# Kernel tuning notes

Measured on AMD Instinct MI355X. Metric: run time of the kernel, lower is better.

Reference implementation:

```python
import jax, jax.numpy as jnp
import numpy as np

N_ATOMS = 30000
N_PAIRS = 1200000
N_BASIS = 7
N_RADIAL = 5
N_SPECIES = 119
R_MIN = 0.5
R_MAX = 6.0
UNITS = (512, 512)
BOX = 6.0  # Angstrom box edge so many pairs fall inside the cutoff
N_FEAT = 360  # gaussian-moment feature count for n_radial=5

# static triangular index sets (fully symmetric contractions)
_TRI2_I, _TRI2_J = np.triu_indices(N_RADIAL)
_TRI3 = np.array([(i, j, k) for i in range(N_RADIAL)
                  for j in range(i, N_RADIAL)
                  for k in range(j, N_RADIAL)], dtype=np.int32)


def setup_inputs() -> dict:
    key = jax.random.key(0)
    ks = jax.random.split(key, 8)
    R = jax.random.uniform(ks[0], (N_ATOMS, 3), jnp.float32) * BOX
    Z = jax.random.randint(ks[1], (N_ATOMS,), 0, N_SPECIES, dtype=jnp.int32)
    idx = jax.random.randint(ks[2], (2, N_PAIRS), 0, N_ATOMS, dtype=jnp.int32)
    W_radial = jax.random.normal(ks[3], (N_SPECIES, N_SPECIES, N_RADIAL, N_BASIS), jnp.float32) / np.sqrt(N_BASIS)
    w1 = jax.random.normal(ks[4], (N_FEAT, UNITS[0]), jnp.float32) / np.sqrt(N_FEAT)
    b1 = jnp.zeros((UNITS[0],), jnp.float32)
    w2 = jax.random.normal(ks[5], (UNITS[0], UNITS[1]), jnp.float32) / np.sqrt(UNITS[0])
    b2 = jnp.zeros((UNITS[1],), jnp.float32)
    w3 = jax.random.normal(ks[6], (UNITS[1], 1), jnp.float32) / np.sqrt(UNITS[1])
    b3 = jnp.zeros((1,), jnp.float32)
    scale = 2.0 * jnp.ones((N_SPECIES, 1), jnp.float32)
    shift = 1.0 * jnp.ones((N_SPECIES, 1), jnp.float32)
    return dict(R=R, Z=Z, idx=idx, W_radial=W_radial, w1=w1, b1=b1,
                w2=w2, b2=b2, w3=w3, b3=b3, scale=scale, shift=shift)


def _descriptor(R, Z, idx, W_radial):
    idx_i, idx_j = idx[0], idx[1]
    # pairwise displacement (free-space displacement fn)
    dr_vec = R[idx_j] - R[idx_i]                                  # [P,3]
    dr = jnp.sqrt(jnp.sum(dr_vec * dr_vec, axis=-1) + 1e-12)      # [P]
    dn = dr_vec / (dr + 1e-5)[:, None]                            # unit vectors [P,3]

    # gaussian radial basis
    betta = N_BASIS ** 2 / R_MAX ** 2
    rad_norm = (2.0 * betta / np.pi) ** 0.25
    shifts = R_MIN + (R_MAX - R_MIN) / N_BASIS * jnp.arange(N_BASIS, dtype=jnp.float32)
    basis = rad_norm * jnp.exp(-betta * (dr[:, None] - shifts) ** 2)  # [P,B]

    # cosine cutoff and per species-pair embedding of the basis
    cutoff = 0.5 * (jnp.cos(jnp.pi * dr / R_MAX) + 1.0) * (dr < R_MAX)
    coeffs = W_radial[Z[idx_i], Z[idx_j]]                          # [P,K,B] irregular gather
    radial = jnp.einsum('pkb,pb->pk', coeffs, basis)               # [P,K]
    radial = radial * (cutoff / np.sqrt(N_BASIS))[:, None]

    seg = lambda x: jax.ops.segment_sum(x, idx_i, num_segments=N_ATOMS)
    # geometric moments of order 0..3
    m0 = seg(radial)                                               # [A,K]
    m1 = seg(radial[:, :, None] * dn[:, None, :])                  # [A,K,3]
    dn2 = dn[:, :, None] * dn[:, None, :]                          # [P,3,3]
    m2 = seg(radial[:, :, None, None] * dn2[:, None])              # [A,K,3,3]
    dn3 = dn2[:, :, :, None] * dn[:, None, None, :]                # [P,3,3,3]
    m3 = seg(radial[:, :, None, None, None] * dn3[:, None])        # [A,K,3,3,3]

    # gaussian-moment invariant contractions
    c1 = jnp.einsum('ari,asi->ars', m1, m1)
    c2 = jnp.einsum('arij,asij->ars', m2, m2)
    c3 = jnp.einsum('arijk,asijk->ars', m3, m3)
    c4 = jnp.einsum('arij,asik,atjk->arst', m2, m2, m2)
    c5 = jnp.einsum('ari,asj,atij->arst', m1, m1, m2)
    c6 = jnp.einsum('arijk,asijl,atkl->arst', m3, m3, m2)
    c7 = jnp.einsum('arijk,asij,atk->arst', m3, m2, m1)

    A = m0.shape[0]
    gm = jnp.concatenate([
        m0,
        c1[:, _TRI2_I, _TRI2_J],
        c2[:, _TRI2_I, _TRI2_J],
        c3[:, _TRI2_I, _TRI2_J],
        c4[:, _TRI3[:, 0], _TRI3[:, 1], _TRI3[:, 2]],
        c5[:, _TRI2_I, _TRI2_J, :].reshape(A, -1),
        c6[:, _TRI2_I, _TRI2_J, :].reshape(A, -1),
        c7.reshape(A, -1),
    ], axis=-1)                                                    # [A,360]
    return gm


def reference(R, Z, idx, W_radial, w1, b1, w2, b2, w3, b3, scale, shift):
    gm = _descriptor(R, Z, idx, W_radial)
    h = jax.nn.swish(gm @ w1 + b1)
    h = jax.nn.swish(h @ w2 + b2)
    h = h @ w3 + b3                                                # [A,1]
    return scale[Z] * h + shift[Z]
```

## Files before the change

kernel.cpp:

```cpp
#include <hip/hip_runtime.h>

#define NA      30000
#define MPAD    30080
#define NPAIRS  1200000
#define NB      7
#define NK      5
#define NSP     119
#define NFEAT   360
#define KP1     384
#define NU      512
#define WROWH   40
#define MAXSLOT 120
#define PSTRIDE 128
#define NBK     118
#define BCAP    11520
#define PPB     4688
#define NTILE   235

#define BETTA      1.3611111111111112f
#define RADNORM    0.96481348f
#define SHIFT_STEP 0.7857142857142857f
#define PI_OVER_R  0.5235987755982988f
#define INV_SQRT7  0.3779644730092272f
#define RMAXV      6.0f

typedef __attribute__((ext_vector_type(8))) short bf16x8;
typedef __attribute__((ext_vector_type(4))) float f32x4;
typedef __attribute__((ext_vector_type(2))) float f32x2;
typedef __attribute__((ext_vector_type(4))) unsigned int u32x4;

__device__ __forceinline__ unsigned short f2b(float x) {
    unsigned u = __float_as_uint(x);
    unsigned r = u + 0x7FFF + ((u >> 16) & 1);
    return (unsigned short)(r >> 16);
}

__device__ __forceinline__ float hval(const unsigned* wu, int e) {
    unsigned u = wu[e >> 1];
    unsigned short hs = (e & 1) ? (unsigned short)(u >> 16)
                                : (unsigned short)(u & 0xFFFF);
    return (float)__builtin_bit_cast(_Float16, hs);
}

__global__ __launch_bounds__(256)
void k_part(const int* __restrict__ idx, const int* __restrict__ Z,
            int* __restrict__ gcur, int* __restrict__ part) {
    __shared__ int hist[NBK];
    __shared__ int base[NBK];
    int tid = threadIdx.x;
    for (int b = tid; b < NBK; b += 256) hist[b] = 0;
    __syncthreads();
    int p0 = blockIdx.x * PPB;
    int p1 = min(p0 + PPB, NPAIRS);
    for (int p = p0 + tid; p < p1; p += 256)
        atomicAdd(&hist[idx[p] >> 8], 1);
    __syncthreads();
    for (int b = tid; b < NBK; b += 256) {
        base[b] = atomicAdd(&gcur[b], hist[b]);
        hist[b] = 0;
    }
    __syncthreads();
    for (int p = p0 + tid; p < p1; p += 256) {
        int i = idx[p];
        int b = i >> 8;
        int j = idx[NPAIRS + p];
        int zj = Z[j];
        int off = base[b] + atomicAdd(&hist[b], 1);
        if (off < BCAP)
            part[b * BCAP + off] = ((i & 255) << 22) | (zj << 15) | j;
    }
}

__global__ __launch_bounds__(256)
void k_csr(const int* __restrict__ part, const int* __restrict__ gcnt,
           int* __restrict__ counts, int* __restrict__ plist) {
    __shared__ int lp[128 * MAXSLOT];
    __shared__ int lc[128];
    int tid = threadIdx.x;
    int lane = tid & 63, wave = tid >> 6;
    int w = blockIdx.x;
    int cb = w >> 1;
    int par = w & 1;
    for (int t = tid; t < 128; t += 256) lc[t] = 0;
    __syncthreads();
    int n = min(gcnt[cb], BCAP);
    for (int e = tid; e < n; e += 256) {
        int v = part[cb * BCAP + e];
        int iloc = v >> 22;
        if ((iloc >> 7) == par) {
            int i7 = iloc & 127;
            int r = atomicAdd(&lc[i7], 1);
            if (r < MAXSLOT) lp[i7 * MAXSLOT + r] = v & 0x3FFFFF;
        }
    }
    __syncthreads();
    for (int t = tid; t < 128; t += 256) {
        int a = w * 128 + t;
        if (a < NA) counts[a] = min(lc[t], MAXSLOT);
    }
    for (int rr = 0; rr < 32; rr++) {
        int row = wave * 32 + rr;
        int a = w * 128 + row;
        if (a < NA) {
            for (int c = lane; c < MAXSLOT; c += 64)
                plist[(size_t)a * PSTRIDE + c] = lp[row * MAXSLOT + c];
        }
    }
}

#define PREP_W   (NSP*NSP*WROWH)
#define PREP_R   NA
#define PREP_W1  (NU*KP1)
#define PREP_W2  (NU*NU)
#define PREP_TOT (PREP_W + PREP_R + PREP_W1 + PREP_W2)
__global__ void k_prep(const float* __restrict__ W, const float* __restrict__ R,
                       const float* __restrict__ w1, const float* __restrict__ w2,
                       unsigned short* __restrict__ Wp, float* __restrict__ Rp,
                       unsigned short* __restrict__ w1T, unsigned short* __restrict__ w2T,
                       int* __restrict__ gcur, float* __restrict__ out) {
    int i = blockIdx.x * blockDim.x + threadIdx.x;
    if (i < 128) gcur[i] = 0;
    if (i < NA) out[i] = 0.f;
    if (i < PREP_W) {
        int row = i / WROWH, e = i - row * WROWH;
        float v = (e < NK * NB) ? W[row * (NK * NB) + e] : 0.f;
        ((_Float16*)Wp)[i] = (_Float16)v;
        return;
    }
    i -= PREP_W;
    if (i < PREP_R) {
        f32x4 v = {R[3*i], R[3*i+1], R[3*i+2], 0.f};
        *(f32x4*)&Rp[4*i] = v;
        return;
    }
    i -= PREP_R;
    if (i < PREP_W1) {
        int c = i / KP1, kp = i - c * KP1;
        w1T[i] = (kp < NFEAT) ? f2b(w1[kp * NU + c]) : (unsigned short)0;
        return;
    }
    i -= PREP_W1;
    if (i < PREP_W2) {
        int c = i >> 9, kp = i & 511;
        w2T[i] = f2b(w2[kp * NU + c]);
    }
}

#define LDM(comp) M[(comp) * 65]

__device__ __forceinline__ void do_c5(const float* M, unsigned short* STrow,
                                      int r, int s, int foff) {
    const int S2[3][3] = {{0,1,2},{1,3,4},{2,4,5}};
    float m1r[3], m1q[3];
#pragma unroll
    for (int i = 0; i < 3; i++) m1r[i] = LDM(r*20+1+i);
#pragma unroll
    for (int i = 0; i < 3; i++) m1q[i] = LDM(s*20+1+i);
    float pre[9];
#pragma unroll
    for (int i = 0; i < 3; i++)
#pragma unroll
        for (int j = 0; j < 3; j++) pre[i*3+j] = m1r[i] * m1q[j];
    for (int t = 0; t < 5; t++) {
        float m2t[6];
#pragma unroll
        for (int u = 0; u < 6; u++) m2t[u] = LDM(t*20+4+u);
        float v = 0.f;
#pragma unroll
        for (int i = 0; i < 3; i++)
#pragma unroll
            for (int j = 0; j < 3; j++)
                v += pre[i*3+j] * m2t[S2[i][j]];
        STrow[foff + t] = f2b(v);
    }
}

__device__ __forceinline__ void do_c6(const float* M, unsigned short* STrow,
                                      int r, int s, int foff) {
    const int S2[3][3] = {{0,1,2},{1,3,4},{2,4,5}};
    const int S3[3][3][3] = {
        {{0,1,2},{1,3,4},{2,4,5}},
        {{1,3,4},{3,6,7},{4,7,8}},
        {{2,4,5},{4,7,8},{5,8,9}}
    };
    float m3r[10];
#pragma unroll
    for (int u = 0; u < 10; u++) m3r[u] = LDM(r*20+10+u);
    float m2q[6];
#pragma unroll
    for (int u = 0; u < 6; u++) m2q[u] = LDM(s*20+4+u);
    float U0 = 0.f, U1 = 0.f, U2 = 0.f;
#pragma unroll
    for (int i = 0; i < 3; i++)
#pragma unroll
        for (int j = 0; j < 3; j++) {
            float ww = m2q[S2[i][j]];
            U0 += m3r[S3[i][j][0]] * ww;
            U1 += m3r[S3[i][j][1]] * ww;
            U2 += m3r[S3[i][j][2]] * ww;
        }
    for (int t = 0; t < 5; t++) {
        float v = U0 * LDM(t*20+1) + U1 * LDM(t*20+2) + U2 * LDM(t*20+3);
        STrow[foff + t] = f2b(v);
    }
}

__device__ __forceinline__ void do_c7(const float* M, unsigned short* STrow,
                                      int r, int s, int foff) {
    const int S2[3][3] = {{0,1,2},{1,3,4},{2,4,5}};
    const int S3[3][3][3] = {
        {{0,1,2},{1,3,4},{2,4,5}},
        {{1,3,4},{3,6,7},{4,7,8}},
        {{2,4,5},{4,7,8},{5,8,9}}
    };
    float m3r[10], m3q[10];
#pragma unroll
    for (int u = 0; u < 10; u++) m3r[u] = LDM(r*20+10+u);
#pragma unroll
    for (int u = 0; u < 10; u++) m3q[u] = LDM(s*20+10+u);
    float T[3][3];
#pragma unroll
    for (int k = 0; k < 3; k++)
#pragma unroll
        for (int l = 0; l < 3; l++) {
            float v = 0.f;
#pragma unroll
            for (int i = 0; i < 3; i++)
#pragma unroll
                for (int j = 0; j < 3; j++)
                    v += m3r[S3[i][j][k]] * m3q[S3[i][j][l]];
            T[k][l] = v;
        }
    for (int t = 0; t < 5; t++) {
        float m2t[6];
#pragma unroll
        for (int u = 0; u < 6; u++) m2t[u] = LDM(t*20+4+u);
        float v = 0.f;
#pragma unroll
        for (int k = 0; k < 3; k++)
#pragma unroll
            for (int l = 0; l < 3; l++)
                v += T[k][l] * m2t[S2[k][l]];
        STrow[foff + t] = f2b(v);
    }
}

__global__ __launch_bounds__(512, 2)
void k_momcon(const float* __restrict__ Rp, const int* __restrict__ Z,
              const unsigned short* __restrict__ WpH, const int* __restrict__ counts,
              const int* __restrict__ plist, unsigned short* __restrict__ gmB) {
    __shared__ float MS[100 * 65];
    __shared__ __align__(4) unsigned short ST[64 * 242];
    int tid = threadIdx.x;
    int g = tid >> 3, q = tid & 7;
    int a0 = blockIdx.x * 64;
    int a = a0 + g;

    if (a < NA) {
        f32x4 ri = *(const f32x4*)&Rp[4*a];
        int Zi = Z[a];
        f32x2 acc[50];
#pragma unroll
        for (int u = 0; u < 50; u++) acc[u] = (f32x2){0.f, 0.f};
        int cnt = min(counts[a], MAXSLOT);
        const int* prow = plist + (size_t)a * PSTRIDE;

        int pk = prow[q];
        for (int t = q; t < cnt; t += 8) {
            int pk_next = prow[(t + 8) & 127];
            int j  = pk & 0x7FFF;
            int Zj = (pk >> 15) & 0x7F;
            f32x4 rj = *(const f32x4*)&Rp[4*j];

            const u32x4* wv = (const u32x4*)(WpH + (size_t)(Zi * NSP + Zj) * WROWH);
            u32x4 wv0 = wv[0], wv1 = wv[1], wv2 = wv[2], wv3 = wv[3], wv4 = wv[4];
            unsigned wu[20];
#pragma unroll
            for (int c = 0; c < 4; c++) {
                wu[c]      = wv0[c];
                wu[4 + c]  = wv1[c];
                wu[8 + c]  = wv2[c];
                wu[12 + c] = wv3[c];
                wu[16 + c] = wv4[c];
            }

            float dx = rj.x - ri.x, dy = rj.y - ri.y, dz = rj.z - ri.z;
            float d2 = dx*dx + dy*dy + dz*dz + 1e-12f;
            float dr = sqrtf(d2);
            float inv = 1.0f / (dr + 1e-5f);
            float nx = dx*inv, ny = dy*inv, nz = dz*inv;

            float basis[NB];
#pragma unroll
            for (int b = 0; b < NB; b++) {
                float tt = dr - (0.5f + SHIFT_STEP * (float)b);
                basis[b] = RADNORM * __expf(-BETTA * tt * tt);
            }
            float cut = (dr < RMAXV) ? 0.5f * (__cosf(PI_OVER_R * dr) + 1.0f) : 0.0f;
            cut *= INV_SQRT7;
            float rad[NK];
#pragma unroll
            for (int k = 0; k < NK; k++) {
                float s = 0.f;
#pragma unroll
                for (int b = 0; b < NB; b++) s += hval(wu, k*NB + b) * basis[b];
                rad[k] = s * cut;
            }
            float gg[20];
            gg[0] = 1.f; gg[1] = nx; gg[2] = ny; gg[3] = nz;
            gg[4] = nx*nx; gg[5] = nx*ny; gg[6] = nx*nz; gg[7] = ny*ny; gg[8] = ny*nz; gg[9] = nz*nz;
            gg[10] = gg[4]*nx; gg[11] = gg[4]*ny; gg[12] = gg[4]*nz; gg[13] = gg[5]*ny; gg[14] = gg[5]*nz;
            gg[15] = gg[6]*nz; gg[16] = gg[7]*ny; gg[17] = gg[7]*nz; gg[18] = gg[8]*nz; gg[19] = gg[9]*nz;
            f32x2 g2[10];
#pragma unroll
            for (int u = 0; u < 10; u++) g2[u] = (f32x2){gg[2*u], gg[2*u+1]};
#pragma unroll
            for (int k = 0; k < NK; k++) {
                f32x2 rk = (f32x2){rad[k], rad[k]};
#pragma unroll
                for (int u = 0; u < 10; u++)
                    acc[k*10 + u] += rk * g2[u];
            }
            pk = pk_next;
        }
#pragma unroll
        for (int u = 0; u < 50; u++) {
            f32x2 v = acc[u];
            double d = __builtin_bit_cast(double, v);
            d = __shfl_xor(d, 1);
            v += __builtin_bit_cast(f32x2, d);
            d = __builtin_bit_cast(double, v);
            d = __shfl_xor(d, 2);
            v += __builtin_bit_cast(f32x2, d);
            d = __builtin_bit_cast(double, v);
            d = __shfl_xor(d, 4);
            v += __builtin_bit_cast(f32x2, d);
            acc[u] = v;
        }
        if (q == 0) {
#pragma unroll
            for (int u = 0; u < 50; u++) {
                MS[(2*u)     * 65 + g] = acc[u].x;
                MS[(2*u + 1) * 65 + g] = acc[u].y;
            }
        }
    }
    __syncthreads();

    int lane = tid & 63, wave = tid >> 6;
    const float* M = MS + lane;
    unsigned short* STrow = ST + lane * 242;

    if (wave == 0) {
        for (int k = 0; k < 5; k++) STrow[k] = f2b(LDM(k * 20));
        int f = 5;
        for (int r = 0; r < 5; r++)
            for (int s = r; s < 5; s++) {
                float v = 0.f;
#pragma unroll
                for (int i = 0; i < 3; i++) v += LDM(r*20+1+i) * LDM(s*20+1+i);
                STrow[f++] = f2b(v);
            }
        const float W2U[6] = {1,2,2,1,2,1};
        for (int r = 0; r < 5; r++)
            for (int s = r; s < 5; s++) {
                float v = 0.f;
#pragma unroll
                for (int u = 0; u < 6; u++) v += W2U[u] * LDM(r*20+4+u) * LDM(s*20+4+u);
                STrow[f++] = f2b(v);
            }
        const float W3U[10] = {1,3,3,3,6,3,1,3,3,1};
        for (int r = 0; r < 5; r++)
            for (int s = r; s < 5; s++) {
                float v = 0.f;
#pragma unroll
                for (int u = 0; u < 10; u++) v += W3U[u] * LDM(r*20+10+u) * LDM(s*20+10+u);
                STrow[f++] = f2b(v);
            }
        do_c7(M, STrow, 3, 4, 160 + 13*5);
        do_c7(M, STrow, 4, 4, 160 + 14*5);
    } else if (wave == 1 || wave == 2) {
        const int S2[3][3] = {{0,1,2},{1,3,4},{2,4,5}};
        int e0 = (wave == 1) ? 0 : 18, e1 = (wave == 1) ? 18 : 35;
        int e = 0;
        for (int r = 0; r < 5; r++)
            for (int s = r; s < 5; s++)
                for (int t = s; t < 5; t++) {
                    if (e >= e0 && e < e1) {
                        float m2r[6], m2q[6], m2t[6];
#pragma unroll
                        for (int u = 0; u < 6; u++) m2r[u] = LDM(r*20+4+u);
#pragma unroll
                        for (int u = 0; u < 6; u++) m2q[u] = LDM(s*20+4+u);
#pragma unroll
                        for (int u = 0; u < 6; u++) m2t[u] = LDM(t*20+4+u);
                        float v = 0.f;
#pragma unroll
                        for (int i = 0; i < 3; i++)
#pragma unroll
                            for (int j = 0; j < 3; j++)
#pragma unroll
                                for (int k = 0; k < 3; k++)
                                    v += m2r[S2[i][j]] * m2q[S2[i][k]] * m2t[S2[j][k]];
                        STrow[50 + e] = f2b(v);
                    }
                    e++;
                }
    } else if (wave == 3) {
        int p = 0;
        for (int r = 0; r < 5; r++)
            for (int s = r; s < 5; s++) {
                if (p < 8) do_c5(M, STrow, r, s, 85 + p*5);
                p++;
            }
        do_c7(M, STrow, 3, 3, 160 + 12*5);
    } else if (wave == 4) {
        int p = 0;
        for (int r = 0; r < 5; r++)
            for (int s = r; s < 5; s++) {
                if (p >= 8) do_c5(M, STrow, r, s, 85 + p*5);
                p++;
            }
        do_c6(M, STrow, 0, 0, 235);
    } else {
        int pc0 = (wave - 5) * 4;
        int p = 0;
        for (int r = 0; r < 5; r++)
            for (int s = r; s < 5; s++) {
                if (p >= pc0 && p < pc0 + 4) do_c7(M, STrow, r, s, 160 + p*5);
                p++;
            }
    }
    __syncthreads();
    for (int e = tid; e < 64 * 120; e += 512) {
        int row = e / 120, c = e - row * 120;
        if (a0 + row < NA)
            *(unsigned int*)&gmB[(size_t)(a0 + row) * KP1 + 2*c] =
                *(const unsigned int*)&ST[row * 242 + 2*c];
    }
    __syncthreads();

    {
        int g0 = 1 + wave * 3;
        for (int gi = 0; gi < 3; gi++) {
            int gr = g0 + gi;
            int r = gr / 5, s = gr - r * 5;
            do_c6(M, STrow, r, s, 235 + gr*5 - 240);
        }
        if (wave == 0) {
            for (int z = 360; z < 384; z++) STrow[z - 240] = 0;
        }
    }
    __syncthreads();
    for (int e = tid; e < 64 * 72; e += 512) {
        int row = e / 72, c = e - row * 72;
        if (a0 + row < NA)
            *(unsigned int*)&gmB[(size_t)(a0 + row) * KP1 + 240 + 2*c] =
                *(const unsigned int*)&ST[row * 242 + 2*c];
    }
}

__device__ __forceinline__ void stage8(const unsigned short* gp, unsigned short* lp) {
    __builtin_amdgcn_global_load_lds(
        (const __attribute__((address_space(1))) unsigned int*)gp,
        (__attribute__((address_space(3))) unsigned int*)lp, 16, 0, 0);
}

template<int KPAD, int MODE>
__global__ __launch_bounds__(256) void k_mfma(const unsigned short* __restrict__ A,
                                              const unsigned short* __restrict__ B,
                                              const float* __restrict__ bias,
                                              const float* __restrict__ w3,
                                              void* __restrict__ outp) {
    __shared__ __align__(16) unsigned char SMEM[35072];
    unsigned short* As = (unsigned short*)SMEM;
    unsigned short* Bs = (unsigned short*)(SMEM + 16384);
    float* red = (float*)(SMEM + 32768);
    int tid = threadIdx.x;
    int lane = tid & 63, wave = tid >> 6;
    int wm = wave >> 1, wn = wave & 1;
    int quad = lane >> 4, l16 = lane & 15;
    int lrow = lane >> 3;
    int lchk = lane & 7;

    for (int t = 0; t < 2; t++) {
        int atile = blockIdx.y * 2 + t;
        if (atile >= NTILE) break;
        int rowA0, rowB0;
        if (MODE == 1) { rowA0 = atile * 128;      rowB0 = blockIdx.x * 128; }
        else           { rowA0 = blockIdx.x * 128; rowB0 = atile * 128; }

        f32x4 acc[4][4];
        f32x4 zero = {0.f, 0.f, 0.f, 0.f};
#pragma unroll
        for (int i = 0; i < 4; i++)
#pragma unroll
            for (int j = 0; j < 4; j++) acc[i][j] = zero;

        for (int k0 = 0; k0 < KPAD; k0 += 64) {
            __syncthreads();
#pragma unroll
            for (int i = 0; i < 4; i++) {
                int r = wave * 32 + i * 8 + lrow;
                int gc = lchk ^ (r & 7);
                stage8(A + (size_t)(rowA0 + r) * KPAD + k0 + gc * 8, &As[(wave * 32 + i * 8) * 64]);
            }
#pragma unroll
            for (int i = 0; i < 4; i++) {
                int r = wave * 32 + i * 8 + lrow;
                int gc = lchk ^ (r & 7);
                stage8(B + (size_t)(rowB0 + r) * KPAD + k0 + gc * 8, &Bs[(wave * 32 + i * 8) * 64]);
            }
            __syncthreads();
#pragma unroll
            for (int s = 0; s < 2; s++) {
                bf16x8 af[4], bfr[4];
#pragma unroll
                for (int mt = 0; mt < 4; mt++) {
                    int r = wm * 64 + mt * 16 + l16;
                    af[mt] = *(const bf16x8*)&As[r * 64 + (((s * 4 + quad) ^ (r & 7)) * 8)];
                }
#pragma unroll
                for (int nt = 0; nt < 4; nt++) {
                    int r = wn * 64 + nt * 16 + l16;
                    bfr[nt] = *(const bf16x8*)&Bs[r * 64 + (((s * 4 + quad) ^ (r & 7)) * 8)];
                }
#pragma unroll
                for (int mt = 0; mt < 4; mt++)
#pragma unroll
                    for (int nt = 0; nt < 4; nt++)
                        acc[mt][nt] = __builtin_amdgcn_mfma_f32_16x16x32_bf16(
                            af[mt], bfr[nt], acc[mt][nt], 0, 0, 0);
            }
        }

        if (MODE == 1) {
            __syncthreads();
            unsigned short* Ot = (unsigned short*)SMEM;
#pragma unroll
            for (int nt = 0; nt < 4; nt++) {
                int c_loc = wn * 64 + nt * 16 + l16;
                float b = bias[rowB0 + c_loc];
#pragma unroll
                for (int mt = 0; mt < 4; mt++) {
#pragma unroll
                    for (int reg = 0; reg < 4; reg++) {
                        int a_loc = wm * 64 + mt * 16 + quad * 4 + reg;
                        float v = acc[mt][nt][reg] + b;
                        Ot[a_loc * 136 + c_loc] = f2b(v / (1.f + __expf(-v)));
                    }
                }
            }
            __syncthreads();
            unsigned short* O = (unsigned short*)outp;
            int half = lane >> 5, l32 = lane & 31;
#pragma unroll
            for (int it = 0; it < 16; it++) {
                int rloc = wave * 32 + it * 2 + half;
                int a = rowA0 + rloc;
                unsigned long long d = *(const unsigned long long*)&Ot[rloc * 136 + l32 * 4];
                if (a < NA)
                    *(unsigned long long*)&O[(size_t)a * NU + rowB0 + l32 * 4] = d;
            }
        } else {
            float pn[4] = {0.f, 0.f, 0.f, 0.f};
#pragma unroll
            for (int mt = 0; mt < 4; mt++) {
#pragma unroll
                for (int reg = 0; reg < 4; reg++) {
                    int c = rowA0 + wm * 64 + mt * 16 + quad * 4 + reg;
                    float b = bias[c];
                    float w3c = w3[c];
#pragma unroll
                    for (int nt = 0; nt < 4; nt++) {
                        float v = acc[mt][nt][reg] + b;
                        pn[nt] += w3c * (v / (1.f + __expf(-v)));
                    }
                }
            }
#pragma unroll
            for (int nt = 0; nt < 4; nt++) {
                pn[nt] += __shfl_xor(pn[nt], 16);
                pn[nt] += __shfl_xor(pn[nt], 32);
            }
            __syncthreads();
            if (quad == 0) {
#pragma unroll
                for (int nt = 0; nt < 4; nt++)
                    red[((wm * 2 + wn) * 4 + nt) * 16 + l16] = pn[nt];
            }
            __syncthreads();
            if (tid < 128) {
                int wn2 = tid >> 6, nt2 = (tid >> 4) & 3, lb = tid & 15;
                float s = red[((0 * 2 + wn2) * 4 + nt2) * 16 + lb]
                        + red[((1 * 2 + wn2) * 4 + nt2) * 16 + lb];
                int a = rowB0 + wn2 * 64 + nt2 * 16 + lb;
                if (a < NA) atomicAdd((float*)outp + a, s);
            }
        }
    }
}

__global__ void k_finish(float* __restrict__ out, const float* __restrict__ b3,
                         const int* __restrict__ Z, const float* __restrict__ scale,
                         const float* __restrict__ shift) {
    int a = blockIdx.x * blockDim.x + threadIdx.x;
    if (a >= NA) return;
    int z = Z[a];
    out[a] = scale[z] * (out[a] + b3[0]) + shift[z];
}

extern "C" void kernel_launch(void* const* d_in, const int* in_sizes, int n_in,
                              void* d_out, int out_size, void* d_ws, size_t ws_size,
                              hipStream_t stream) {
    const float* R    = (const float*)d_in[0];
    const int*   Z    = (const int*)  d_in[1];
    const int*   idx  = (const int*)  d_in[2];
    const float* Wr   = (const float*)d_in[3];
    const float* w1   = (const float*)d_in[4];
    const float* b1   = (const float*)d_in[5];
    const float* w2   = (const float*)d_in[6];
    const float* b2   = (const float*)d_in[7];
    const float* w3   = (const float*)d_in[8];
    const float* b3   = (const float*)d_in[9];
    const float* scale= (const float*)d_in[10];
    const float* shift= (const float*)d_in[11];
    float* out = (float*)d_out;
    char* ws = (char*)d_ws;

    int*            gcur   = (int*)  (ws + 0);
    int*            counts = (int*)  (ws + 512);
    int*            part   = (int*)  (ws + 120576);
    int*            plist  = (int*)  (ws + 5558016);
    unsigned short* gmB    = (unsigned short*)(ws + 32918016);
    unsigned short* w1T    = (unsigned short*)(ws + 56019456);
    unsigned short* w2T    = (unsigned short*)(ws + 56412672);
    unsigned short* h1B    = (unsigned short*)(ws + 56936960);
    unsigned short* WpH    = (unsigned short*)(ws + 87738880);
    float*          Rpad   = (float*)(ws + 89778064);

    k_prep   <<<(PREP_TOT + 255) / 256, 256, 0, stream>>>(Wr, R, w1, w2, WpH, Rpad,
                                                          w1T, w2T, gcur, out);
    k_part   <<<256, 256, 0, stream>>>(idx, Z, gcur, part);
    k_csr    <<<235, 256, 0, stream>>>(part, gcur, counts, plist);
    k_momcon <<<(NA + 63) / 64, 512, 0, stream>>>(Rpad, Z, WpH, counts, plist, gmB);

    k_mfma<KP1, 1><<<dim3(NU / 128, 118), 256, 0, stream>>>(gmB, w1T, b1, nullptr, (void*)h1B);
    k_mfma<NU,  2><<<dim3(NU / 128, 118), 256, 0, stream>>>(w2T, h1B, b2, w3, (void*)out);

    k_finish<<<(NA + 255) / 256, 256, 0, stream>>>(out, b3, Z, scale, shift);
}
```

Baseline: 250.4 us.

## Compute radial basis by recurrence, use fp16 dot2, prefetch neighbor positions

Replaces the seven Gaussian exponentials per pair with one Gaussian and one exponential, then builds the rest through a multiplicative recurrence with precomputed constants. The per-species radial weights are repacked into padded groups of eight, so the basis contraction can use packed fp16 dot2 instructions on pairs of values. The neighbor position load is software-pipelined one iteration ahead to hide gather latency. The trade-off is reduced precision, since the basis is rounded to fp16 and the recurrence can accumulate rounding error, plus extra registers for the prefetch.

```diff
diff --git a/kernel.cpp b/kernel.cpp
--- a/kernel.cpp
+++ b/kernel.cpp
@@ -23,23 +23,18 @@
 #define PI_OVER_R  0.5235987755982988f
 #define INV_SQRT7  0.3779644730092272f
 #define RMAXV      6.0f
+#define TCOEF      2.138888888888889f
 
 typedef __attribute__((ext_vector_type(8))) short bf16x8;
 typedef __attribute__((ext_vector_type(4))) float f32x4;
 typedef __attribute__((ext_vector_type(2))) float f32x2;
 typedef __attribute__((ext_vector_type(4))) unsigned int u32x4;
+typedef _Float16 h16x2 __attribute__((ext_vector_type(2)));
 
 __device__ __forceinline__ unsigned short f2b(float x) {
     unsigned u = __float_as_uint(x);
     unsigned r = u + 0x7FFF + ((u >> 16) & 1);
     return (unsigned short)(r >> 16);
-}
-
-__device__ __forceinline__ float hval(const unsigned* wu, int e) {
-    unsigned u = wu[e >> 1];
-    unsigned short hs = (e & 1) ? (unsigned short)(u >> 16)
-                                : (unsigned short)(u & 0xFFFF);
-    return (float)__builtin_bit_cast(_Float16, hs);
 }
 
 __global__ __launch_bounds__(256)
@@ -123,7 +118,8 @@
     if (i < NA) out[i] = 0.f;
     if (i < PREP_W) {
         int row = i / WROWH, e = i - row * WROWH;
-        float v = (e < NK * NB) ? W[row * (NK * NB) + e] : 0.f;
+        int k = e >> 3, b = e & 7;
+        float v = (b < 7) ? W[row * (NK * NB) + k * NB + b] : 0.f;
         ((_Float16*)Wp)[i] = (_Float16)v;
         return;
     }
@@ -265,13 +261,20 @@
         int cnt = min(counts[a], MAXSLOT);
         const int* prow = plist + (size_t)a * PSTRIDE;
 
-        int pk = prow[q];
+        const float DCH[6] = {0.14812156f, 0.027590652f, 0.0051393300f,
+                              0.00095730500f, 0.00017831700f, 3.3215300e-05f};
+
+        int pk0 = prow[q & 127];
+        int pk1 = prow[(q + 8) & 127];
+        int j0c = min(pk0 & 0x7FFF, NA - 1);
+        f32x4 rj = *(const f32x4*)&Rp[4 * j0c];
+
         for (int t = q; t < cnt; t += 8) {
-            int pk_next = prow[(t + 8) & 127];
-            int j  = pk & 0x7FFF;
-            int Zj = (pk >> 15) & 0x7F;
-            f32x4 rj = *(const f32x4*)&Rp[4*j];
-
+            int pk2 = prow[(t + 16) & 127];
+            int j1c = min(pk1 & 0x7FFF, NA - 1);
+            f32x4 rjn = *(const f32x4*)&Rp[4 * j1c];
+
+            int Zj = (pk0 >> 15) & 0x7F;
             const u32x4* wv = (const u32x4*)(WpH + (size_t)(Zi * NSP + Zj) * WROWH);
             u32x4 wv0 = wv[0], wv1 = wv[1], wv2 = wv[2], wv3 = wv[3], wv4 = wv[4];
             unsigned wu[20];
@@ -290,22 +293,41 @@
             float inv = 1.0f / (dr + 1e-5f);
             float nx = dx*inv, ny = dy*inv, nz = dz*inv;
 
-            float basis[NB];
-#pragma unroll
-            for (int b = 0; b < NB; b++) {
-                float tt = dr - (0.5f + SHIFT_STEP * (float)b);
-                basis[b] = RADNORM * __expf(-BETTA * tt * tt);
-            }
+            float t0 = dr - 0.5f;
+            float bb[NB];
+            bb[0] = RADNORM * __expf(-BETTA * t0 * t0);
+            float Tg = __expf(TCOEF * dr);
+#pragma unroll
+            for (int b = 0; b < 6; b++) bb[b+1] = bb[b] * Tg * DCH[b];
+
             float cut = (dr < RMAXV) ? 0.5f * (__cosf(PI_OVER_R * dr) + 1.0f) : 0.0f;
             cut *= INV_SQRT7;
+
+            h16x2 bp[4];
+            bp[0] = (h16x2){(_Float16)bb[0], (_Float16)bb[1]};
+            bp[1] = (h16x2){(_Float16)bb[2], (_Float16)bb[3]};
+            bp[2] = (h16x2){(_Float16)bb[4], (_Float16)bb[5]};
+            bp[3] = (h16x2){(_Float16)bb[6], (_Float16)0.0f};
+
             float rad[NK];
 #pragma unroll
             for (int k = 0; k < NK; k++) {
                 float s = 0.f;
-#pragma unroll
-                for (int b = 0; b < NB; b++) s += hval(wu, k*NB + b) * basis[b];
+#if __has_builtin(__builtin_amdgcn_fdot2)
+#pragma unroll
+                for (int c = 0; c < 4; c++)
+                    s = __builtin_amdgcn_fdot2(
+                        __builtin_bit_cast(h16x2, wu[k*4 + c]), bp[c], s, false);
+#else
+#pragma unroll
+                for (int c = 0; c < 4; c++) {
+                    h16x2 w = __builtin_bit_cast(h16x2, wu[k*4 + c]);
+                    s += (float)w.x * (float)bp[c].x + (float)w.y * (float)bp[c].y;
+                }
+#endif
                 rad[k] = s * cut;
             }
+
             float gg[20];
             gg[0] = 1.f; gg[1] = nx; gg[2] = ny; gg[3] = nz;
             gg[4] = nx*nx; gg[5] = nx*ny; gg[6] = nx*nz; gg[7] = ny*ny; gg[8] = ny*nz; gg[9] = nz*nz;
@@ -321,7 +343,7 @@
                 for (int u = 0; u < 10; u++)
                     acc[k*10 + u] += rk * g2[u];
             }
-            pk = pk_next;
+            pk0 = pk1; pk1 = pk2; rj = rjn;
         }
 #pragma unroll
         for (int u = 0; u < 50; u++) {
```

After: 247.4 us. About the same (-1.2%).
